# Kernel optimization log

Measured on AMD Instinct MI355X. Metric: run time of the kernel, lower is better.

## Reference

```python
import jax, jax.numpy as jnp
import numpy as np

B, S, T, E, H = 2, 2048, 2048, 1024, 16
HD = E // H  # head_dim = 64


def setup_inputs() -> dict:
    key = jax.random.key(0)
    ks = jax.random.split(key, 12)
    sc = 1.0 / np.sqrt(E)
    inp = {
        "query": jax.random.normal(ks[0], (B, S, E), jnp.float32),
        "key": jax.random.normal(ks[1], (B, T, E), jnp.float32),
        "value": jax.random.normal(ks[2], (B, T, E), jnp.float32),
        "attn_mask": jnp.ones((S, T), jnp.int32),
        # nn.Linear params: y = x @ W.T + b
        "Wq": jax.random.normal(ks[3], (E, E), jnp.float32) * sc,
        "bq": jax.random.normal(ks[4], (E,), jnp.float32) * sc,
        "Wk": jax.random.normal(ks[5], (E, E), jnp.float32) * sc,
        "bk": jax.random.normal(ks[6], (E,), jnp.float32) * sc,
        "Wv": jax.random.normal(ks[7], (E, E), jnp.float32) * sc,
        "bv": jax.random.normal(ks[8], (E,), jnp.float32) * sc,
        "Wo": jax.random.normal(ks[9], (E, E), jnp.float32) * sc,
        "bo": jax.random.normal(ks[10], (E,), jnp.float32) * sc,
    }
    return inp


def reference(query, key, value, attn_mask, Wq, bq, Wk, bk, Wv, bv, Wo, bo):
    N, Sq, Ed = query.shape
    Tk = key.shape[1]
    # projections (torch Linear: x @ W.T + b)
    q = query @ Wq.T + bq
    k = key @ Wk.T + bk
    v = value @ Wv.T + bv
    # split heads -> (N, H, S, HD)
    q = q.reshape(N, Sq, H, HD).transpose(0, 2, 1, 3)
    k = k.reshape(N, Tk, H, HD).transpose(0, 2, 1, 3)
    v = v.reshape(N, Tk, H, HD).transpose(0, 2, 1, 3)
    # scaled dot-product scores: (N, H, S, T)
    energy = jnp.einsum("nhsd,nhtd->nhst", q, k) / jnp.sqrt(jnp.float32(HD))
    energy = jnp.where(attn_mask[None, None, :, :] == 0, -jnp.inf, energy)
    attn = jax.nn.softmax(energy, axis=3)
    # dropout is identity in eval mode
    out = jnp.einsum("nhst,nhtd->nshd", attn, v).reshape(N, Sq, Ed)
    return out @ Wo.T + bo
```

## Files before the change

### kernel.cpp

```cpp
#include <hip/hip_runtime.h>

typedef __attribute__((ext_vector_type(8))) short short8;
typedef __attribute__((ext_vector_type(4))) float f32x4;
typedef __attribute__((ext_vector_type(16))) float f32x16;

#define DEV __device__ __forceinline__

constexpr int Bb = 2, Ss = 2048, Tt = 2048, Ee = 1024, Hh = 16, HDd = 64;
constexpr int Mm = Bb * Ss;
constexpr size_t NX = (size_t)Mm * Ee;
constexpr size_t NW = (size_t)Ee * Ee;

constexpr size_t OFF_XQ   = 0;
constexpr size_t OFF_XK   = OFF_XQ + NX * 2;
constexpr size_t OFF_XV   = OFF_XK + NX * 2;
constexpr size_t OFF_WQ   = OFF_XV + NX * 2;
constexpr size_t OFF_WK   = OFF_WQ + NW * 2;
constexpr size_t OFF_WV   = OFF_WK + NW * 2;
constexpr size_t OFF_WO   = OFF_WV + NW * 2;
constexpr size_t OFF_QH   = OFF_WO + NW * 2;
constexpr size_t OFF_KH   = OFF_QH + NX * 2;
constexpr size_t OFF_VH   = OFF_KH + NX * 2;
constexpr size_t OFF_OB   = OFF_VH + NX * 2;
constexpr size_t OFF_FLAG = OFF_OB + NX * 2;

DEV unsigned short f2bf(float f) {
  union { float f; unsigned u; } v; v.f = f;
  unsigned r = v.u + 0x7fffu + ((v.u >> 16) & 1u);
  return (unsigned short)(r >> 16);
}

#define GLDS16(g, l) __builtin_amdgcn_global_load_lds(                         \
    (const __attribute__((address_space(1))) void*)(g),                        \
    (__attribute__((address_space(3))) void*)(l), 16, 0, 0)

#define PLSWAP(a, b) asm("v_permlane32_swap_b32 %0, %1" : "+v"(a), "+v"(b))
#define CVTPK(d, lo, hi_) asm("v_cvt_pk_bf16_f32 %0, %1, %2" : "=v"(d) : "v"(lo), "v"(hi_))

#if __has_builtin(__builtin_amdgcn_exp2f)
#define EXP2(x) __builtin_amdgcn_exp2f(x)
#else
#define EXP2(x) __expf((x) * 0.69314718f)
#endif

constexpr float SCLQ = 0.18033688f;

__global__ __launch_bounds__(256) void prep_kernel(
    const float* __restrict__ q, const float* __restrict__ k, const float* __restrict__ v,
    const float* __restrict__ wq, const float* __restrict__ wk,
    const float* __restrict__ wv, const float* __restrict__ wo,
    const int* __restrict__ mask,
    unsigned short* __restrict__ Xq, unsigned short* __restrict__ Xk, unsigned short* __restrict__ Xv,
    unsigned short* __restrict__ Wqb, unsigned short* __restrict__ Wkb,
    unsigned short* __restrict__ Wvb, unsigned short* __restrict__ Wob,
    int* __restrict__ flagZero)
{
  constexpr size_t NXv = NX / 4, NWv = NW / 4;
  constexpr size_t tot = 4 * NXv + 4 * NWv;
  for (size_t u = (size_t)blockIdx.x * blockDim.x + threadIdx.x; u < tot;
       u += (size_t)gridDim.x * blockDim.x) {
    if (u < 3 * NXv) {
      const float* src; unsigned short* dst; size_t off;
      if (u < NXv)            { src = q; dst = Xq; off = u; }
      else if (u < 2 * NXv)   { src = k; dst = Xk; off = u - NXv; }
      else                    { src = v; dst = Xv; off = u - 2 * NXv; }
      float4 f = ((const float4*)src)[off];
      ushort4 o; o.x = f2bf(f.x); o.y = f2bf(f.y); o.z = f2bf(f.z); o.w = f2bf(f.w);
      ((ushort4*)dst)[off] = o;
    } else if (u < 3 * NXv + 4 * NWv) {
      size_t uu = u - 3 * NXv;
      int wsel = (int)(uu / NWv); size_t off = uu % NWv;
      const float* src = wsel == 0 ? wq : wsel == 1 ? wk : wsel == 2 ? wv : wo;
      unsigned short* dst = wsel == 0 ? Wqb : wsel == 1 ? Wkb : wsel == 2 ? Wvb : Wob;
      float4 f = ((const float4*)src)[off];
      ushort4 o; o.x = f2bf(f.x); o.y = f2bf(f.y); o.z = f2bf(f.z); o.w = f2bf(f.w);
      ((ushort4*)dst)[off] = o;
    } else {
      size_t off = u - 3 * NXv - 4 * NWv;
      int4 m = ((const int4*)mask)[off];
      if (m.x == 0 || m.y == 0 || m.z == 0 || m.w == 0) *flagZero = 1;
    }
  }
}

DEV void gemm128(const unsigned short* __restrict__ A, const unsigned short* __restrict__ Bm,
                 unsigned short (*Asm)[128 * 32], unsigned short (*Bsm)[128 * 32],
                 f32x4 acc[4][4], int K)
{
  const int t = threadIdx.x;
  const int w = t >> 6, lane = t & 63;
  const int l15 = lane & 15, l4 = lane >> 4;
  const int wm = w >> 1, wn = w & 1;
  const int srow = lane >> 2;
  const int skc  = (lane & 3) * 8;
#pragma unroll
  for (int mi = 0; mi < 4; ++mi)
#pragma unroll
    for (int ni = 0; ni < 4; ++ni) acc[mi][ni] = (f32x4){0.f, 0.f, 0.f, 0.f};

#define GSTAGE(d, k0)                                                              \
  {                                                                                \
    GLDS16(A  + (size_t)(w * 16 + srow) * K + (k0) + skc,      Asm[d] + w * 512);  \
    GLDS16(A  + (size_t)(64 + w * 16 + srow) * K + (k0) + skc, Asm[d] + 2048 + w * 512); \
    GLDS16(Bm + (size_t)(w * 16 + srow) * K + (k0) + skc,      Bsm[d] + w * 512);  \
    GLDS16(Bm + (size_t)(64 + w * 16 + srow) * K + (k0) + skc, Bsm[d] + 2048 + w * 512); \
  }

  GSTAGE(0, 0)
  int it = 0;
  for (int k0 = 0; k0 < K; k0 += 32, ++it) {
    const int cur = it & 1;
    asm volatile("s_waitcnt vmcnt(0)" ::: "memory");
    __builtin_amdgcn_s_barrier();
    if (k0 + 32 < K) GSTAGE(cur ^ 1, k0 + 32)

    short8 af[4], bf[4];
#pragma unroll
    for (int mi = 0; mi < 4; ++mi)
      af[mi] = *(const short8*)&Asm[cur][(wm * 64 + mi * 16 + l15) * 32 + l4 * 8];
#pragma unroll
    for (int ni = 0; ni < 4; ++ni)
      bf[ni] = *(const short8*)&Bsm[cur][(wn * 64 + ni * 16 + l15) * 32 + l4 * 8];
    __builtin_amdgcn_s_setprio(1);
#pragma unroll
    for (int mi = 0; mi < 4; ++mi)
#pragma unroll
      for (int ni = 0; ni < 4; ++ni)
        acc[mi][ni] = __builtin_amdgcn_mfma_f32_16x16x32_bf16(af[mi], bf[ni], acc[mi][ni], 0, 0, 0);
    __builtin_amdgcn_s_setprio(0);
  }
#undef GSTAGE
}

DEV void gemm128_8w(const unsigned short* __restrict__ A, const unsigned short* __restrict__ Bm,
                    unsigned short (*Asm)[128 * 32], unsigned short (*Bsm)[128 * 32],
                    f32x4 acc[2][4], int K)
{
  const int tid = threadIdx.x, w = tid >> 6, lane = tid & 63;
  const int l15 = lane & 15, l4 = lane >> 4;
  const int wm = w >> 1, wn = w & 1;
  const int grow = tid >> 2, gk = (tid & 3) * 8;
#pragma unroll
  for (int mi = 0; mi < 2; ++mi)
#pragma unroll
    for (int ni = 0; ni < 4; ++ni) acc[mi][ni] = (f32x4){0.f, 0.f, 0.f, 0.f};

#define GSTAGE8(d, k0)                                                   \
  {                                                                      \
    GLDS16(A  + (size_t)grow * K + (k0) + gk, Asm[d] + w * 512);         \
    GLDS16(Bm + (size_t)grow * K + (k0) + gk, Bsm[d] + w * 512);         \
  }

  GSTAGE8(0, 0)
  int it = 0;
  for (int k0 = 0; k0 < K; k0 += 32, ++it) {
    const int cur = it & 1;
    asm volatile("s_waitcnt vmcnt(0)" ::: "memory");
    __builtin_amdgcn_s_barrier();
    if (k0 + 32 < K) GSTAGE8(cur ^ 1, k0 + 32)

    short8 af[2], bf[4];
#pragma unroll
    for (int mi = 0; mi < 2; ++mi)
      af[mi] = *(const short8*)&Asm[cur][(wm * 32 + mi * 16 + l15) * 32 + l4 * 8];
#pragma unroll
    for (int ni = 0; ni < 4; ++ni)
      bf[ni] = *(const short8*)&Bsm[cur][(wn * 64 + ni * 16 + l15) * 32 + l4 * 8];
    __builtin_amdgcn_s_setprio(1);
#pragma unroll
    for (int mi = 0; mi < 2; ++mi)
#pragma unroll
      for (int ni = 0; ni < 4; ++ni)
        acc[mi][ni] = __builtin_amdgcn_mfma_f32_16x16x32_bf16(af[mi], bf[ni], acc[mi][ni], 0, 0, 0);
    __builtin_amdgcn_s_setprio(0);
  }
#undef GSTAGE8
}

__global__ __launch_bounds__(256, 4) void gemm_qkv(
    const unsigned short* __restrict__ Xq, const unsigned short* __restrict__ Xk,
    const unsigned short* __restrict__ Xv,
    const unsigned short* __restrict__ Wqb, const unsigned short* __restrict__ Wkb,
    const unsigned short* __restrict__ Wvb,
    const float* __restrict__ bq, const float* __restrict__ bk, const float* __restrict__ bv,
    unsigned short* __restrict__ Qh, unsigned short* __restrict__ Kh, unsigned short* __restrict__ Vh)
{
  __shared__ unsigned short Asm[2][128 * 32], Bsm[2][128 * 32];
  const int orig = (blockIdx.z * 32 + blockIdx.y) * 8 + blockIdx.x;
  const int sid  = (orig & 7) * 96 + (orig >> 3);
  const int z  = sid >> 8;
  const int by = (sid & 255) >> 3, bx = sid & 7;
  const unsigned short* A  = (z == 0) ? Xq  : (z == 1) ? Xk  : Xv;
  const unsigned short* Bw = (z == 0) ? Wqb : (z == 1) ? Wkb : Wvb;
  const float* bias        = (z == 0) ? bq  : (z == 1) ? bk  : bv;
  unsigned short* Out      = (z == 0) ? Qh  : (z == 1) ? Kh  : Vh;
  f32x4 acc[4][4];
  gemm128(A + (size_t)by * 128 * Ee, Bw + (size_t)bx * 128 * Ee, Asm, Bsm, acc, Ee);
  const int t = threadIdx.x, w = t >> 6, lane = t & 63, l15 = lane & 15, l4 = lane >> 4;
  const int wm = w >> 1, wn = w & 1;
  if (z < 2) {
    const float osc = (z == 0) ? SCLQ : 1.0f;
#pragma unroll
    for (int ni = 0; ni < 4; ++ni) {
      int col = bx * 128 + wn * 64 + ni * 16 + l15;
      float bcol = bias[col];
      int h = col >> 6, hd = col & 63;
#pragma unroll
      for (int mi = 0; mi < 4; ++mi) {
#pragma unroll
        for (int r = 0; r < 4; ++r) {
          int row = by * 128 + wm * 64 + mi * 16 + l4 * 4 + r;
          int b = row >> 11, s = row & 2047;
          Out[(((size_t)(b * Hh + h)) * Ss + s) * HDd + hd] = f2bf((acc[mi][ni][r] + bcol) * osc);
        }
      }
    }
  } else {
#pragma unroll
    for (int ni = 0; ni < 4; ++ni) {
      int col = bx * 128 + wn * 64 + ni * 16 + l15;
      float bcol = bias[col];
      int h = col >> 6, hd = col & 63;
#pragma unroll
      for (int mi = 0; mi < 4; ++mi) {
        int row = by * 128 + wm * 64 + mi * 16 + l4 * 4;
        int b = row >> 11, s = row & 2047;
        ushort4 pk;
        pk.x = f2bf(acc[mi][ni][0] + bcol); pk.y = f2bf(acc[mi][ni][1] + bcol);
        pk.z = f2bf(acc[mi][ni][2] + bcol); pk.w = f2bf(acc[mi][ni][3] + bcol);
        *(ushort4*)&Out[((size_t)((b * Hh + h) * HDd + hd)) * Ss + s] = pk;
      }
    }
  }
}

__global__ __launch_bounds__(512) void gemm_out(
    const unsigned short* __restrict__ Ob, const unsigned short* __restrict__ Wob,
    const float* __restrict__ bo, float* __restrict__ out)
{
  __shared__ unsigned short Asm[2][128 * 32], Bsm[2][128 * 32];
  const int orig = blockIdx.y * 8 + blockIdx.x;
  const int sid  = (orig & 7) * 32 + (orig >> 3);
  const int by = sid >> 3, bx = sid & 7;
  f32x4 acc[2][4];
  gemm128_8w(Ob + (size_t)by * 128 * Ee, Wob + (size_t)bx * 128 * Ee, Asm, Bsm, acc, Ee);
  const int tid = threadIdx.x, w = tid >> 6, lane = tid & 63;
  const int l15 = lane & 15, l4 = lane >> 4;
  const int wm = w >> 1, wn = w & 1;
#pragma unroll
  for (int ni = 0; ni < 4; ++ni) {
    int col = bx * 128 + wn * 64 + ni * 16 + l15;
    float bcol = bo[col];
#pragma unroll
    for (int mi = 0; mi < 2; ++mi) {
#pragma unroll
      for (int r = 0; r < 4; ++r) {
        int row = by * 128 + wm * 32 + mi * 16 + l4 * 4 + r;
        out[(size_t)row * Ee + col] = acc[mi][ni][r] + bcol;
      }
    }
  }
}

__global__ __launch_bounds__(256, 4) void attn_kernel(
    const unsigned short* __restrict__ Qh, const unsigned short* __restrict__ Kh,
    const unsigned short* __restrict__ Vh, const int* __restrict__ mask,
    const int* __restrict__ flagZero, unsigned short* __restrict__ Ob)
{
  __shared__ unsigned short Ks[2][64 * 64];
  __shared__ unsigned short Vs[2][64 * 64];
  const int bh = blockIdx.y, qt = blockIdx.x;
  const int tid = threadIdx.x, w = tid >> 6, lane = tid & 63;
  const int l31 = lane & 31, hi = lane >> 5;
  const int g = w >> 1, p = w & 1;
  const bool useMask = (*flagZero != 0);
  const size_t bhBase = (size_t)bh * Ss * HDd;
  const int s0 = qt * 64 + g * 32;
  const int trow = p * 32 + l31;

  short8 qf[4];
#pragma unroll
  for (int ks = 0; ks < 4; ++ks)
    qf[ks] = *(const short8*)&Qh[bhBase + (size_t)(s0 + l31) * 64 + ks * 16 + hi * 8];

  f32x16 o0, o1, Z16;
#pragma unroll
  for (int r = 0; r < 16; ++r) { o0[r] = 0.f; o1[r] = 0.f; Z16[r] = 0.f; }
  float l_r = 0.f;

  const int cRow = tid >> 3, cG = (tid & 7) ^ (cRow & 7);

#define STAGE(d, kt2)                                                                         \
  {                                                                                           \
    _Pragma("unroll")                                                                         \
    for (int i = 0; i < 2; ++i)                                                               \
      GLDS16(Kh + bhBase + (size_t)((kt2) + i * 32 + cRow) * 64 + cG * 8,                     \
             &Ks[d][0] + (i * 256 + w * 64) * 8);                                             \
    _Pragma("unroll")                                                                         \
    for (int i = 0; i < 2; ++i)                                                               \
      GLDS16(Vh + bhBase + (size_t)(i * 32 + cRow) * Ss + (kt2) + cG * 8,                     \
             &Vs[d][0] + (i * 256 + w * 64) * 8);                                             \
  }

#define SMPACK(kt2)                                                                           \
  {                                                                                           \
    if (useMask) {                                                                            \
      int sg = s0 + l31;                                                                      \
      _Pragma("unroll")                                                                       \
      for (int r = 0; r < 16; ++r) {                                                          \
        int tg = (kt2) + p * 32 + (r & 3) + 8 * (r >> 2) + 4 * hi;                            \
        if (mask[(size_t)sg * Tt + tg] == 0) pr[r] = -1e30f;                                  \
      }                                                                                       \
    }                                                                                         \
    _Pragma("unroll")                                                                         \
    for (int r = 0; r < 16; ++r) pr[r] = EXP2(pr[r]);                                         \
    float a0 = (pr[0] + pr[1]) + (pr[2] + pr[3]);                                             \
    float a1 = (pr[4] + pr[5]) + (pr[6] + pr[7]);                                             \
    float a2 = (pr[8] + pr[9]) + (pr[10] + pr[11]);                                           \
    float a3 = (pr[12] + pr[13]) + (pr[14] + pr[15]);                                         \
    l_r += (a0 + a1) + (a2 + a3);                                                             \
    _Pragma("unroll")                                                                         \
    for (int h2 = 0; h2 < 2; ++h2) {                                                          \
      unsigned c0, c1, d0, d1; const int bse = h2 * 8;                                        \
      CVTPK(c0, pr[bse + 0], pr[bse + 1]);                                                    \
      CVTPK(c1, pr[bse + 2], pr[bse + 3]);                                                    \
      CVTPK(d0, pr[bse + 4], pr[bse + 5]);                                                    \
      CVTPK(d1, pr[bse + 6], pr[bse + 7]);                                                    \
      PLSWAP(c0, d0); PLSWAP(c1, d1);                                                         \
      union { unsigned u[4]; short8 s; } cc;                                                  \
      cc.u[0] = c0; cc.u[1] = c1; cc.u[2] = d0; cc.u[3] = d1;                                 \
      pa[h2] = cc.s;                                                                          \
    }                                                                                         \
  }

  f32x16 pr;
  short8 pa[2];

  STAGE(0, 0)
  asm volatile("s_waitcnt vmcnt(2)" ::: "memory");
  __builtin_amdgcn_s_barrier();
  STAGE(1, 64)
  {
    const unsigned short* Kc = &Ks[0][0];
    short8 ka = *(const short8*)&Kc[trow * 64 + ((hi ^ (l31 & 7)) * 8)];
    pr = __builtin_amdgcn_mfma_f32_32x32x16_bf16(ka, qf[0], Z16, 0, 0, 0);
#pragma unroll
    for (int ks = 1; ks < 4; ++ks) {
      short8 kb = *(const short8*)&Kc[trow * 64 + (((ks * 2 + hi) ^ (l31 & 7)) * 8)];
      pr = __builtin_amdgcn_mfma_f32_32x32x16_bf16(kb, qf[ks], pr, 0, 0, 0);
    }
  }
  SMPACK(0)

  for (int t = 0; t < 32; ++t) {
    const int cur = t & 1;
    if (t < 31) { asm volatile("s_waitcnt vmcnt(2)" ::: "memory"); }
    else        { asm volatile("s_waitcnt vmcnt(0)" ::: "memory"); }
    __builtin_amdgcn_s_barrier();

    const unsigned short* Vc = &Vs[cur][0];
    __builtin_amdgcn_s_setprio(1);
    if (t < 31) {
      const unsigned short* Kn = &Ks[cur ^ 1][0];
      short8 ka0 = *(const short8*)&Kn[trow * 64 + (((0 + hi) ^ (l31 & 7)) * 8)];
      short8 ka1 = *(const short8*)&Kn[trow * 64 + (((2 + hi) ^ (l31 & 7)) * 8)];
      short8 ka2 = *(const short8*)&Kn[trow * 64 + (((4 + hi) ^ (l31 & 7)) * 8)];
      short8 ka3 = *(const short8*)&Kn[trow * 64 + (((6 + hi) ^ (l31 & 7)) * 8)];
      short8 vf00 = *(const short8*)&Vc[l31 * 64 + (((p * 4 + 0 + hi) ^ (l31 & 7)) * 8)];
      short8 vf01 = *(const short8*)&Vc[(32 + l31) * 64 + (((p * 4 + 0 + hi) ^ ((l31 & 7))) * 8)];
      short8 vf10 = *(const short8*)&Vc[l31 * 64 + (((p * 4 + 2 + hi) ^ (l31 & 7)) * 8)];
      short8 vf11 = *(const short8*)&Vc[(32 + l31) * 64 + (((p * 4 + 2 + hi) ^ ((l31 & 7))) * 8)];
      f32x16 prN;
      prN = __builtin_amdgcn_mfma_f32_32x32x16_bf16(ka0, qf[0], Z16, 0, 0, 0);
      o0  = __builtin_amdgcn_mfma_f32_32x32x16_bf16(pa[0], vf00, o0, 0, 0, 0);
      o1  = __builtin_amdgcn_mfma_f32_32x32x16_bf16(pa[0], vf01, o1, 0, 0, 0);
      prN = __builtin_amdgcn_mfma_f32_32x32x16_bf16(ka1, qf[1], prN, 0, 0, 0);
      o0  = __builtin_amdgcn_mfma_f32_32x32x16_bf16(pa[1], vf10, o0, 0, 0, 0);
      prN = __builtin_amdgcn_mfma_f32_32x32x16_bf16(ka2, qf[2], prN, 0, 0, 0);
      o1  = __builtin_amdgcn_mfma_f32_32x32x16_bf16(pa[1], vf11, o1, 0, 0, 0);
      prN = __builtin_amdgcn_mfma_f32_32x32x16_bf16(ka3, qf[3], prN, 0, 0, 0);
      pr = prN;
    } else {
      short8 vf00 = *(const short8*)&Vc[l31 * 64 + (((p * 4 + 0 + hi) ^ (l31 & 7)) * 8)];
      short8 vf01 = *(const short8*)&Vc[(32 + l31) * 64 + (((p * 4 + 0 + hi) ^ ((l31 & 7))) * 8)];
      short8 vf10 = *(const short8*)&Vc[l31 * 64 + (((p * 4 + 2 + hi) ^ (l31 & 7)) * 8)];
      short8 vf11 = *(const short8*)&Vc[(32 + l31) * 64 + (((p * 4 + 2 + hi) ^ ((l31 & 7))) * 8)];
      o0 = __builtin_amdgcn_mfma_f32_32x32x16_bf16(pa[0], vf00, o0, 0, 0, 0);
      o1 = __builtin_amdgcn_mfma_f32_32x32x16_bf16(pa[0], vf01, o1, 0, 0, 0);
      o0 = __builtin_amdgcn_mfma_f32_32x32x16_bf16(pa[1], vf10, o0, 0, 0, 0);
      o1 = __builtin_amdgcn_mfma_f32_32x32x16_bf16(pa[1], vf11, o1, 0, 0, 0);
    }
    __builtin_amdgcn_s_setprio(0);

    if (t < 31) SMPACK((t + 1) * 64)

    __builtin_amdgcn_s_barrier();
    if (t < 30) STAGE(cur, (t + 2) * 64)
  }
#undef STAGE
#undef SMPACK

  __syncthreads();

  float* Ox = (float*)&Ks[0][0];
  float* Ml = (float*)&Vs[0][0];
  float lt = l_r + __shfl_xor(l_r, 32);
  if (p == 1) {
#pragma unroll
    for (int r = 0; r < 16; ++r) {
      int sr = (r & 3) + 8 * (r >> 2) + 4 * hi;
      Ox[g * 2048 + sr * 64 + l31]      = o0[r];
      Ox[g * 2048 + sr * 64 + 32 + l31] = o1[r];
    }
    if (hi == 0) Ml[g * 32 + l31] = lt;
  }
  __syncthreads();
  if (p == 0) {
    const int b = bh >> 4, h = bh & 15;
    float ltot = lt + Ml[g * 32 + l31];
    float linv = ltot > 0.f ? 1.0f / ltot : 0.f;
#pragma unroll
    for (int r = 0; r < 16; ++r) {
      int sr = (r & 3) + 8 * (r >> 2) + 4 * hi;
      float li = __shfl(linv, sr);
      size_t rowbase = (size_t)(b * Ss + s0 + sr) * Ee + h * 64;
      Ob[rowbase + l31]      = f2bf((o0[r] + Ox[g * 2048 + sr * 64 + l31]) * li);
      Ob[rowbase + 32 + l31] = f2bf((o1[r] + Ox[g * 2048 + sr * 64 + 32 + l31]) * li);
    }
  }
}

extern "C" void kernel_launch(void* const* d_in, const int* in_sizes, int n_in,
                              void* d_out, int out_size, void* d_ws, size_t ws_size,
                              hipStream_t stream) {
  const float* q   = (const float*)d_in[0];
  const float* k   = (const float*)d_in[1];
  const float* v   = (const float*)d_in[2];
  const int*  msk  = (const int*)d_in[3];
  const float* Wq  = (const float*)d_in[4];
  const float* bq  = (const float*)d_in[5];
  const float* Wk  = (const float*)d_in[6];
  const float* bk  = (const float*)d_in[7];
  const float* Wv  = (const float*)d_in[8];
  const float* bv  = (const float*)d_in[9];
  const float* Wo  = (const float*)d_in[10];
  const float* bo  = (const float*)d_in[11];
  float* out = (float*)d_out;

  char* ws = (char*)d_ws;
  unsigned short* Xq  = (unsigned short*)(ws + OFF_XQ);
  unsigned short* Xk  = (unsigned short*)(ws + OFF_XK);
  unsigned short* Xv  = (unsigned short*)(ws + OFF_XV);
  unsigned short* Wqb = (unsigned short*)(ws + OFF_WQ);
  unsigned short* Wkb = (unsigned short*)(ws + OFF_WK);
  unsigned short* Wvb = (unsigned short*)(ws + OFF_WV);
  unsigned short* Wob = (unsigned short*)(ws + OFF_WO);
  unsigned short* Qh  = (unsigned short*)(ws + OFF_QH);
  unsigned short* Kh  = (unsigned short*)(ws + OFF_KH);
  unsigned short* Vh  = (unsigned short*)(ws + OFF_VH);
  unsigned short* Ob  = (unsigned short*)(ws + OFF_OB);
  int* flagZero       = (int*)(ws + OFF_FLAG);

  hipMemsetAsync(flagZero, 0, 4, stream);
  prep_kernel<<<4096, 256, 0, stream>>>(q, k, v, Wq, Wk, Wv, Wo, msk,
                                        Xq, Xk, Xv, Wqb, Wkb, Wvb, Wob, flagZero);
  gemm_qkv<<<dim3(8, 32, 3), 256, 0, stream>>>(Xq, Xk, Xv, Wqb, Wkb, Wvb,
                                               bq, bk, bv, Qh, Kh, Vh);
  attn_kernel<<<dim3(32, 32), 256, 0, stream>>>(Qh, Kh, Vh, msk, flagZero, Ob);
  gemm_out<<<dim3(8, 32), 512, 0, stream>>>(Ob, Wob, bo, out);
}
```

Measured before the change: 127.5 us.

## Fuse fp32-to-bf16 activation conversion into QKV GEMM A-tile loading

Removes the separate conversion of query/key/value to bf16 in the prep kernel. The QKV GEMM now loads fp32 A tiles into registers, converts them with packed bf16 instructions, and writes them to LDS, while B still streams via direct global-to-LDS loads. This eliminates a full write and re-read of the bf16 activation copies. In exchange, the GEMM reads twice as many A bytes per tile, uses more registers (occupancy hint lowered to 3), and adds an extra barrier per k-step.

```diff
diff --git a/kernel.cpp b/kernel.cpp
--- a/kernel.cpp
+++ b/kernel.cpp
@@ -46,46 +46,35 @@
 constexpr float SCLQ = 0.18033688f;
 
 __global__ __launch_bounds__(256) void prep_kernel(
-    const float* __restrict__ q, const float* __restrict__ k, const float* __restrict__ v,
     const float* __restrict__ wq, const float* __restrict__ wk,
     const float* __restrict__ wv, const float* __restrict__ wo,
     const int* __restrict__ mask,
-    unsigned short* __restrict__ Xq, unsigned short* __restrict__ Xk, unsigned short* __restrict__ Xv,
     unsigned short* __restrict__ Wqb, unsigned short* __restrict__ Wkb,
     unsigned short* __restrict__ Wvb, unsigned short* __restrict__ Wob,
     int* __restrict__ flagZero)
 {
-  constexpr size_t NXv = NX / 4, NWv = NW / 4;
-  constexpr size_t tot = 4 * NXv + 4 * NWv;
+  constexpr size_t NWv = NW / 4, NXv = NX / 4;
+  constexpr size_t tot = 4 * NWv + NXv;
   for (size_t u = (size_t)blockIdx.x * blockDim.x + threadIdx.x; u < tot;
        u += (size_t)gridDim.x * blockDim.x) {
-    if (u < 3 * NXv) {
-      const float* src; unsigned short* dst; size_t off;
-      if (u < NXv)            { src = q; dst = Xq; off = u; }
-      else if (u < 2 * NXv)   { src = k; dst = Xk; off = u - NXv; }
-      else                    { src = v; dst = Xv; off = u - 2 * NXv; }
-      float4 f = ((const float4*)src)[off];
-      ushort4 o; o.x = f2bf(f.x); o.y = f2bf(f.y); o.z = f2bf(f.z); o.w = f2bf(f.w);
-      ((ushort4*)dst)[off] = o;
-    } else if (u < 3 * NXv + 4 * NWv) {
-      size_t uu = u - 3 * NXv;
-      int wsel = (int)(uu / NWv); size_t off = uu % NWv;
+    if (u < 4 * NWv) {
+      int wsel = (int)(u / NWv); size_t off = u % NWv;
       const float* src = wsel == 0 ? wq : wsel == 1 ? wk : wsel == 2 ? wv : wo;
       unsigned short* dst = wsel == 0 ? Wqb : wsel == 1 ? Wkb : wsel == 2 ? Wvb : Wob;
       float4 f = ((const float4*)src)[off];
       ushort4 o; o.x = f2bf(f.x); o.y = f2bf(f.y); o.z = f2bf(f.z); o.w = f2bf(f.w);
       ((ushort4*)dst)[off] = o;
     } else {
-      size_t off = u - 3 * NXv - 4 * NWv;
+      size_t off = u - 4 * NWv;
       int4 m = ((const int4*)mask)[off];
       if (m.x == 0 || m.y == 0 || m.z == 0 || m.w == 0) *flagZero = 1;
     }
   }
 }
 
-DEV void gemm128(const unsigned short* __restrict__ A, const unsigned short* __restrict__ Bm,
-                 unsigned short (*Asm)[128 * 32], unsigned short (*Bsm)[128 * 32],
-                 f32x4 acc[4][4], int K)
+DEV void gemm128_f32A(const float* __restrict__ Af, const unsigned short* __restrict__ Bm,
+                      unsigned short (*Asm)[128 * 32], unsigned short (*Bsm)[128 * 32],
+                      f32x4 acc[4][4], int K)
 {
   const int t = threadIdx.x;
   const int w = t >> 6, lane = t & 63;
@@ -93,26 +82,44 @@
   const int wm = w >> 1, wn = w & 1;
   const int srow = lane >> 2;
   const int skc  = (lane & 3) * 8;
+  const int ar = t >> 2;
+  const int ak = (t & 3) * 8;
 #pragma unroll
   for (int mi = 0; mi < 4; ++mi)
 #pragma unroll
     for (int ni = 0; ni < 4; ++ni) acc[mi][ni] = (f32x4){0.f, 0.f, 0.f, 0.f};
 
-#define GSTAGE(d, k0)                                                              \
-  {                                                                                \
-    GLDS16(A  + (size_t)(w * 16 + srow) * K + (k0) + skc,      Asm[d] + w * 512);  \
-    GLDS16(A  + (size_t)(64 + w * 16 + srow) * K + (k0) + skc, Asm[d] + 2048 + w * 512); \
-    GLDS16(Bm + (size_t)(w * 16 + srow) * K + (k0) + skc,      Bsm[d] + w * 512);  \
-    GLDS16(Bm + (size_t)(64 + w * 16 + srow) * K + (k0) + skc, Bsm[d] + 2048 + w * 512); \
-  }
-
-  GSTAGE(0, 0)
+  float4 a0, a1, a2, a3;
+#define ALOAD(k0)                                                            \
+  { const float* ap  = Af + (size_t)ar * K + (k0) + ak;                      \
+    const float* ap2 = ap + (size_t)64 * K;                                  \
+    a0 = *(const float4*)ap;  a1 = *(const float4*)(ap + 4);                 \
+    a2 = *(const float4*)ap2; a3 = *(const float4*)(ap2 + 4); }
+#define BSTAGE(d, k0)                                                        \
+  { GLDS16(Bm + (size_t)(w * 16 + srow) * K + (k0) + skc,      Bsm[d] + w * 512);        \
+    GLDS16(Bm + (size_t)(64 + w * 16 + srow) * K + (k0) + skc, Bsm[d] + 2048 + w * 512); }
+#define AWRITE(d)                                                            \
+  { unsigned u0, u1, u2, u3, u4, u5, u6, u7;                                 \
+    CVTPK(u0, a0.x, a0.y); CVTPK(u1, a0.z, a0.w);                            \
+    CVTPK(u2, a1.x, a1.y); CVTPK(u3, a1.z, a1.w);                            \
+    CVTPK(u4, a2.x, a2.y); CVTPK(u5, a2.z, a2.w);                            \
+    CVTPK(u6, a3.x, a3.y); CVTPK(u7, a3.z, a3.w);                            \
+    union { unsigned u[4]; short8 s; } p0, p1;                               \
+    p0.u[0] = u0; p0.u[1] = u1; p0.u[2] = u2; p0.u[3] = u3;                  \
+    p1.u[0] = u4; p1.u[1] = u5; p1.u[2] = u6; p1.u[3] = u7;                  \
+    *(short8*)&Asm[d][ar * 32 + ak]        = p0.s;                           \
+    *(short8*)&Asm[d][(64 + ar) * 32 + ak] = p1.s; }
+
+  ALOAD(0) BSTAGE(0, 0)
+  asm volatile("s_waitcnt vmcnt(0)" ::: "memory");
+  AWRITE(0)
+  __syncthreads();
+
   int it = 0;
   for (int k0 = 0; k0 < K; k0 += 32, ++it) {
     const int cur = it & 1;
-    asm volatile("s_waitcnt vmcnt(0)" ::: "memory");
-    __builtin_amdgcn_s_barrier();
-    if (k0 + 32 < K) GSTAGE(cur ^ 1, k0 + 32)
+    const bool more = (k0 + 32 < K);
+    if (more) { ALOAD(k0 + 32) BSTAGE(cur ^ 1, k0 + 32) }
 
     short8 af[4], bf[4];
 #pragma unroll
@@ -128,8 +135,16 @@
       for (int ni = 0; ni < 4; ++ni)
         acc[mi][ni] = __builtin_amdgcn_mfma_f32_16x16x32_bf16(af[mi], bf[ni], acc[mi][ni], 0, 0, 0);
     __builtin_amdgcn_s_setprio(0);
-  }
-#undef GSTAGE
+
+    if (more) {
+      asm volatile("s_waitcnt vmcnt(0)" ::: "memory");
+      AWRITE(cur ^ 1)
+    }
+    __syncthreads();
+  }
+#undef ALOAD
+#undef BSTAGE
+#undef AWRITE
 }
 
 DEV void gemm128_8w(const unsigned short* __restrict__ A, const unsigned short* __restrict__ Bm,
@@ -177,9 +192,8 @@
 #undef GSTAGE8
 }
 
-__global__ __launch_bounds__(256, 4) void gemm_qkv(
-    const unsigned short* __restrict__ Xq, const unsigned short* __restrict__ Xk,
-    const unsigned short* __restrict__ Xv,
+__global__ __launch_bounds__(256, 3) void gemm_qkv(
+    const float* __restrict__ q, const float* __restrict__ k, const float* __restrict__ v,
     const unsigned short* __restrict__ Wqb, const unsigned short* __restrict__ Wkb,
     const unsigned short* __restrict__ Wvb,
     const float* __restrict__ bq, const float* __restrict__ bk, const float* __restrict__ bv,
@@ -190,12 +204,12 @@
   const int sid  = (orig & 7) * 96 + (orig >> 3);
   const int z  = sid >> 8;
   const int by = (sid & 255) >> 3, bx = sid & 7;
-  const unsigned short* A  = (z == 0) ? Xq  : (z == 1) ? Xk  : Xv;
+  const float* A           = (z == 0) ? q   : (z == 1) ? k   : v;
   const unsigned short* Bw = (z == 0) ? Wqb : (z == 1) ? Wkb : Wvb;
   const float* bias        = (z == 0) ? bq  : (z == 1) ? bk  : bv;
   unsigned short* Out      = (z == 0) ? Qh  : (z == 1) ? Kh  : Vh;
   f32x4 acc[4][4];
-  gemm128(A + (size_t)by * 128 * Ee, Bw + (size_t)bx * 128 * Ee, Asm, Bsm, acc, Ee);
+  gemm128_f32A(A + (size_t)by * 128 * Ee, Bw + (size_t)bx * 128 * Ee, Asm, Bsm, acc, Ee);
   const int t = threadIdx.x, w = t >> 6, lane = t & 63, l15 = lane & 15, l4 = lane >> 4;
   const int wm = w >> 1, wn = w & 1;
   if (z < 2) {
@@ -448,9 +462,6 @@
   float* out = (float*)d_out;
 
   char* ws = (char*)d_ws;
-  unsigned short* Xq  = (unsigned short*)(ws + OFF_XQ);
-  unsigned short* Xk  = (unsigned short*)(ws + OFF_XK);
-  unsigned short* Xv  = (unsigned short*)(ws + OFF_XV);
   unsigned short* Wqb = (unsigned short*)(ws + OFF_WQ);
   unsigned short* Wkb = (unsigned short*)(ws + OFF_WK);
   unsigned short* Wvb = (unsigned short*)(ws + OFF_WV);
@@ -462,9 +473,9 @@
   int* flagZero       = (int*)(ws + OFF_FLAG);
 
   hipMemsetAsync(flagZero, 0, 4, stream);
-  prep_kernel<<<4096, 256, 0, stream>>>(q, k, v, Wq, Wk, Wv, Wo, msk,
-                                        Xq, Xk, Xv, Wqb, Wkb, Wvb, Wob, flagZero);
-  gemm_qkv<<<dim3(8, 32, 3), 256, 0, stream>>>(Xq, Xk, Xv, Wqb, Wkb, Wvb,
+  prep_kernel<<<2048, 256, 0, stream>>>(Wq, Wk, Wv, Wo, msk,
+                                        Wqb, Wkb, Wvb, Wob, flagZero);
+  gemm_qkv<<<dim3(8, 32, 3), 256, 0, stream>>>(q, k, v, Wqb, Wkb, Wvb,
                                                bq, bk, bv, Qh, Kh, Vh);
   attn_kernel<<<dim3(32, 32), 256, 0, stream>>>(Qh, Kh, Vh, msk, flagZero, Ob);
   gemm_out<<<dim3(8, 32), 512, 0, stream>>>(Ob, Wob, bo, out);
```

Result: faster. 122.0 us (-4.4%).

## Run QKV GEMM with 8 waves per tile and remap attention blocks across XCDs

Applied to the files above, without the earlier changes.

The QKV projection GEMM now uses the existing 8-wave (512-thread) 128x128 tile routine in place of the 4-wave one. Each wave holds half as many accumulators, which lowers register pressure and raises the number of waves available to hide latency. Separately, the attention kernel's block index is remapped so that consecutive hardware block IDs, which are dispatched round-robin across XCDs, share batch-heads. This is meant to keep each head's K/V data within one XCD's L2. The risks are extra LDS-load instructions per MFMA in the GEMM and a possible change in load balance.

```diff
diff --git a/kernel.cpp b/kernel.cpp
--- a/kernel.cpp
+++ b/kernel.cpp
@@ -83,55 +83,6 @@
   }
 }
 
-DEV void gemm128(const unsigned short* __restrict__ A, const unsigned short* __restrict__ Bm,
-                 unsigned short (*Asm)[128 * 32], unsigned short (*Bsm)[128 * 32],
-                 f32x4 acc[4][4], int K)
-{
-  const int t = threadIdx.x;
-  const int w = t >> 6, lane = t & 63;
-  const int l15 = lane & 15, l4 = lane >> 4;
-  const int wm = w >> 1, wn = w & 1;
-  const int srow = lane >> 2;
-  const int skc  = (lane & 3) * 8;
-#pragma unroll
-  for (int mi = 0; mi < 4; ++mi)
-#pragma unroll
-    for (int ni = 0; ni < 4; ++ni) acc[mi][ni] = (f32x4){0.f, 0.f, 0.f, 0.f};
-
-#define GSTAGE(d, k0)                                                              \
-  {                                                                                \
-    GLDS16(A  + (size_t)(w * 16 + srow) * K + (k0) + skc,      Asm[d] + w * 512);  \
-    GLDS16(A  + (size_t)(64 + w * 16 + srow) * K + (k0) + skc, Asm[d] + 2048 + w * 512); \
-    GLDS16(Bm + (size_t)(w * 16 + srow) * K + (k0) + skc,      Bsm[d] + w * 512);  \
-    GLDS16(Bm + (size_t)(64 + w * 16 + srow) * K + (k0) + skc, Bsm[d] + 2048 + w * 512); \
-  }
-
-  GSTAGE(0, 0)
-  int it = 0;
-  for (int k0 = 0; k0 < K; k0 += 32, ++it) {
-    const int cur = it & 1;
-    asm volatile("s_waitcnt vmcnt(0)" ::: "memory");
-    __builtin_amdgcn_s_barrier();
-    if (k0 + 32 < K) GSTAGE(cur ^ 1, k0 + 32)
-
-    short8 af[4], bf[4];
-#pragma unroll
-    for (int mi = 0; mi < 4; ++mi)
-      af[mi] = *(const short8*)&Asm[cur][(wm * 64 + mi * 16 + l15) * 32 + l4 * 8];
-#pragma unroll
-    for (int ni = 0; ni < 4; ++ni)
-      bf[ni] = *(const short8*)&Bsm[cur][(wn * 64 + ni * 16 + l15) * 32 + l4 * 8];
-    __builtin_amdgcn_s_setprio(1);
-#pragma unroll
-    for (int mi = 0; mi < 4; ++mi)
-#pragma unroll
-      for (int ni = 0; ni < 4; ++ni)
-        acc[mi][ni] = __builtin_amdgcn_mfma_f32_16x16x32_bf16(af[mi], bf[ni], acc[mi][ni], 0, 0, 0);
-    __builtin_amdgcn_s_setprio(0);
-  }
-#undef GSTAGE
-}
-
 DEV void gemm128_8w(const unsigned short* __restrict__ A, const unsigned short* __restrict__ Bm,
                     unsigned short (*Asm)[128 * 32], unsigned short (*Bsm)[128 * 32],
                     f32x4 acc[2][4], int K)
@@ -177,7 +128,7 @@
 #undef GSTAGE8
 }
 
-__global__ __launch_bounds__(256, 4) void gemm_qkv(
+__global__ __launch_bounds__(512) void gemm_qkv(
     const unsigned short* __restrict__ Xq, const unsigned short* __restrict__ Xk,
     const unsigned short* __restrict__ Xv,
     const unsigned short* __restrict__ Wqb, const unsigned short* __restrict__ Wkb,
@@ -194,9 +145,10 @@
   const unsigned short* Bw = (z == 0) ? Wqb : (z == 1) ? Wkb : Wvb;
   const float* bias        = (z == 0) ? bq  : (z == 1) ? bk  : bv;
   unsigned short* Out      = (z == 0) ? Qh  : (z == 1) ? Kh  : Vh;
-  f32x4 acc[4][4];
-  gemm128(A + (size_t)by * 128 * Ee, Bw + (size_t)bx * 128 * Ee, Asm, Bsm, acc, Ee);
-  const int t = threadIdx.x, w = t >> 6, lane = t & 63, l15 = lane & 15, l4 = lane >> 4;
+  f32x4 acc[2][4];
+  gemm128_8w(A + (size_t)by * 128 * Ee, Bw + (size_t)bx * 128 * Ee, Asm, Bsm, acc, Ee);
+  const int tid = threadIdx.x, w = tid >> 6, lane = tid & 63;
+  const int l15 = lane & 15, l4 = lane >> 4;
   const int wm = w >> 1, wn = w & 1;
   if (z < 2) {
     const float osc = (z == 0) ? SCLQ : 1.0f;
@@ -206,10 +158,10 @@
       float bcol = bias[col];
       int h = col >> 6, hd = col & 63;
 #pragma unroll
-      for (int mi = 0; mi < 4; ++mi) {
+      for (int mi = 0; mi < 2; ++mi) {
 #pragma unroll
         for (int r = 0; r < 4; ++r) {
-          int row = by * 128 + wm * 64 + mi * 16 + l4 * 4 + r;
+          int row = by * 128 + wm * 32 + mi * 16 + l4 * 4 + r;
           int b = row >> 11, s = row & 2047;
           Out[(((size_t)(b * Hh + h)) * Ss + s) * HDd + hd] = f2bf((acc[mi][ni][r] + bcol) * osc);
         }
@@ -222,8 +174,8 @@
       float bcol = bias[col];
       int h = col >> 6, hd = col & 63;
 #pragma unroll
-      for (int mi = 0; mi < 4; ++mi) {
-        int row = by * 128 + wm * 64 + mi * 16 + l4 * 4;
+      for (int mi = 0; mi < 2; ++mi) {
+        int row = by * 128 + wm * 32 + mi * 16 + l4 * 4;
         int b = row >> 11, s = row & 2047;
         ushort4 pk;
         pk.x = f2bf(acc[mi][ni][0] + bcol); pk.y = f2bf(acc[mi][ni][1] + bcol);
@@ -269,7 +221,10 @@
 {
   __shared__ unsigned short Ks[2][64 * 64];
   __shared__ unsigned short Vs[2][64 * 64];
-  const int bh = blockIdx.y, qt = blockIdx.x;
+  const int orig = blockIdx.y * 32 + blockIdx.x;
+  const int slot = orig >> 3;
+  const int bh = (orig & 7) * 4 + (slot >> 5);
+  const int qt = slot & 31;
   const int tid = threadIdx.x, w = tid >> 6, lane = tid & 63;
   const int l31 = lane & 31, hi = lane >> 5;
   const int g = w >> 1, p = w & 1;
@@ -464,7 +419,7 @@
   hipMemsetAsync(flagZero, 0, 4, stream);
   prep_kernel<<<4096, 256, 0, stream>>>(q, k, v, Wq, Wk, Wv, Wo, msk,
                                         Xq, Xk, Xv, Wqb, Wkb, Wvb, Wob, flagZero);
-  gemm_qkv<<<dim3(8, 32, 3), 256, 0, stream>>>(Xq, Xk, Xv, Wqb, Wkb, Wvb,
+  gemm_qkv<<<dim3(8, 32, 3), 512, 0, stream>>>(Xq, Xk, Xv, Wqb, Wkb, Wvb,
                                                bq, bk, bv, Qh, Kh, Vh);
   attn_kernel<<<dim3(32, 32), 256, 0, stream>>>(Qh, Kh, Vh, msk, flagZero, Ob);
   gemm_out<<<dim3(8, 32), 512, 0, stream>>>(Ob, Wob, bo, out);
```

Result: no change. 127.9 us (+0.3%).
